# Optimization experiments

Hardware: AMD Instinct MI355X
Metric: run time of the kernel (lower is better)

## Reference

```python
import jax, jax.numpy as jnp
import numpy as np

DIM = 2048
N_HEADS = 16
KV_LORA = 512
NOPE = 128
ROPE = 64
V_DIM = 128
QK_DIM = NOPE + ROPE  # 192
B, S = 2, 2048
ROPE_THETA = 10000.0
ROPE_FACTOR = 40.0
BETA_FAST, BETA_SLOW = 32, 1
ORIG_LEN, MAX_LEN = 4096, 16384
MSCALE_ARG = 1.0
EPS = 1e-6


def _precompute_freqs(seqlen):
    # DeepSeek YaRN-corrected rotary frequencies (interleaved-pair convention).
    d = ROPE
    freqs = 1.0 / (ROPE_THETA ** (np.arange(0, d, 2, dtype=np.float64) / d))
    if MAX_LEN > ORIG_LEN:
        def corr_dim(n_rot):
            return d * np.log(ORIG_LEN / (n_rot * 2 * np.pi)) / (2 * np.log(ROPE_THETA))
        low = max(int(np.floor(corr_dim(BETA_FAST))), 0)
        high = min(int(np.ceil(corr_dim(BETA_SLOW))), d - 1)
        smooth = 1.0 - np.clip((np.arange(d // 2) - low) / max(high - low, 1e-3), 0, 1)
        freqs = freqs / ROPE_FACTOR * (1 - smooth) + freqs * smooth
    t = np.arange(seqlen, dtype=np.float64)
    ang = np.outer(t, freqs)  # [S, d/2]
    return np.cos(ang).astype(np.float32), np.sin(ang).astype(np.float32)


def softmax_scale():
    scale = QK_DIM ** -0.5
    if MAX_LEN > ORIG_LEN:
        m = 0.1 * MSCALE_ARG * float(np.log(ROPE_FACTOR)) + 1.0
        scale = scale * m * m
    return scale


def setup_inputs() -> dict:
    key = jax.random.key(0)
    ks = jax.random.split(key, 6)
    w_std = 0.02
    fc, fs = _precompute_freqs(S)
    return {
        "x": jax.random.normal(ks[0], (B, S, DIM), jnp.float32),
        "wq": jax.random.normal(ks[1], (N_HEADS * QK_DIM, DIM), jnp.float32) * w_std,
        "wkv_a": jax.random.normal(ks[2], (KV_LORA + ROPE, DIM), jnp.float32) * w_std,
        "kv_norm_w": jnp.ones((KV_LORA,), jnp.float32),
        "wkv_b": jax.random.normal(ks[3], (N_HEADS * (NOPE + V_DIM), KV_LORA), jnp.float32) * w_std,
        "wo": jax.random.normal(ks[4], (DIM, N_HEADS * V_DIM), jnp.float32) * w_std,
        "freqs_cos": jnp.asarray(fc),
        "freqs_sin": jnp.asarray(fs),
    }


def _apply_rotary(x, cos, sin):
    # x: [B, S, H, d]; interleaved complex pairs, cos/sin: [S, d/2]
    xr = x.reshape(*x.shape[:-1], -1, 2)
    x_re, x_im = xr[..., 0], xr[..., 1]
    c = cos[None, :, None, :]
    s = sin[None, :, None, :]
    y_re = x_re * c - x_im * s
    y_im = x_re * s + x_im * c
    return jnp.stack((y_re, y_im), axis=-1).reshape(x.shape)


def _rmsnorm(x, w):
    return x * jax.lax.rsqrt(jnp.mean(x * x, axis=-1, keepdims=True) + EPS) * w


def reference(x, wq, wkv_a, kv_norm_w, wkv_b, wo, freqs_cos, freqs_sin):
    b, s, _ = x.shape
    # Q projection (q_lora_rank == 0 path)
    q = (x @ wq.T).reshape(b, s, N_HEADS, QK_DIM)
    q_nope, q_pe = q[..., :NOPE], q[..., NOPE:]
    q_pe = _apply_rotary(q_pe, freqs_cos, freqs_sin)
    # Low-rank KV compression
    kv = x @ wkv_a.T  # [B, S, 512+64]
    kv_c, k_pe = kv[..., :KV_LORA], kv[..., KV_LORA:]
    k_pe = _apply_rotary(k_pe[:, :, None, :], freqs_cos, freqs_sin)  # [B,S,1,64]
    kv_c = _rmsnorm(kv_c, kv_norm_w)
    kvb = (kv_c @ wkv_b.T).reshape(b, s, N_HEADS, NOPE + V_DIM)
    k_nope, v = kvb[..., :NOPE], kvb[..., NOPE:]
    k = jnp.concatenate([k_nope, jnp.broadcast_to(k_pe, (b, s, N_HEADS, ROPE))], axis=-1)
    # Causal attention
    scores = jnp.einsum("bshd,bthd->bhst", q, k) * softmax_scale()
    causal = jnp.tril(jnp.ones((s, s), bool))
    scores = jnp.where(causal[None, None], scores, jnp.float32(-1e30))
    p = jax.nn.softmax(scores, axis=-1)
    out = jnp.einsum("bhst,bthd->bshd", p, v).reshape(b, s, N_HEADS * V_DIM)
    return out @ wo.T
```

## Files before the change

kernel.cpp:

```cpp
#include <hip/hip_runtime.h>
#include <math.h>

#define NH      16
#define D_NOPE  128
#define D_ROPE  64
#define D_QK    192
#define D_V     128
#define KV_LORA 512
#define NB      2
#define SEQ     2048
#define NTOK    (NB*SEQ)
#define QROW    (NH*D_QK)
#define KVBROW  (NH*(D_NOPE+D_V))
#define EPSF    1e-6f

typedef unsigned short u16;
typedef float  floatx4 __attribute__((ext_vector_type(4)));
typedef __bf16 bf16x8  __attribute__((ext_vector_type(8)));
typedef u16    u16x4   __attribute__((ext_vector_type(4)));
typedef u16    u16x8   __attribute__((ext_vector_type(8)));

__device__ __forceinline__ u16 f2bf(float f) {
    unsigned u = __builtin_bit_cast(unsigned, f);
    return (u16)((u + 0x7fffu + ((u >> 16) & 1u)) >> 16);
}

__device__ __forceinline__ void async_copy16(const void* g, void* l) {
    __builtin_amdgcn_global_load_lds(
        (const __attribute__((address_space(1))) unsigned int*)g,
        (__attribute__((address_space(3))) unsigned int*)l,
        16, 0, 0);
}

__global__ __launch_bounds__(256) void cast_bf16(const float* __restrict__ in,
                                                 u16* __restrict__ out) {
    const int i = (blockIdx.x * 256 + threadIdx.x) * 4;
    const float4 v = *(const float4*)&in[i];
    u16x4 o; o[0] = f2bf(v.x); o[1] = f2bf(v.y); o[2] = f2bf(v.z); o[3] = f2bf(v.w);
    *(u16x4*)&out[i] = o;
}

__global__ __launch_bounds__(256) void cast_pad_wkva(const float* __restrict__ in,
                                                     u16* __restrict__ out) {
    const int i = (blockIdx.x * 256 + threadIdx.x) * 4;
    const int r = i >> 11;
    u16x4 o;
    if (r < 576) {
        const float4 v = *(const float4*)&in[i];
        o[0] = f2bf(v.x); o[1] = f2bf(v.y); o[2] = f2bf(v.z); o[3] = f2bf(v.w);
    } else {
        o[0] = 0; o[1] = 0; o[2] = 0; o[3] = 0;
    }
    *(u16x4*)&out[i] = o;
}

template<int MODE>
__global__ __launch_bounds__(256) void gemm_mfma(const u16* __restrict__ A,
                                                 const u16* __restrict__ B,
                                                 void* __restrict__ Cout,
                                                 u16* __restrict__ kbuf,
                                                 u16* __restrict__ vT,
                                                 int M, int N, int K) {
    __shared__ u16 As[128 * 32];
    __shared__ u16 Bs[128 * 32];
    const int tid  = threadIdx.x;
    const int wave = tid >> 6, lane = tid & 63;
    const int m0 = blockIdx.y * 128, n0 = blockIdx.x * 128;
    const int wm = (wave & 1) * 64, wn = (wave >> 1) * 64;

    const int srow = wave * 32 + (lane >> 2);
    const int kch  = (lane & 3) * 8;
    const u16* gA0 = A + (size_t)(m0 + srow) * K + kch;
    const u16* gA1 = gA0 + (size_t)16 * K;
    const u16* gB0 = B + (size_t)(n0 + srow) * K + kch;
    const u16* gB1 = gB0 + (size_t)16 * K;
    u16* lA0 = &As[(wave * 32) * 32];
    u16* lA1 = &As[(wave * 32 + 16) * 32];
    u16* lB0 = &Bs[(wave * 32) * 32];
    u16* lB1 = &Bs[(wave * 32 + 16) * 32];

    floatx4 acc[4][4];
#pragma unroll
    for (int i = 0; i < 4; ++i)
#pragma unroll
        for (int j = 0; j < 4; ++j) acc[i][j] = 0.f;

    const int lrow = lane & 15;
    const int lkh  = (lane >> 4) * 8;

    for (int k0 = 0; k0 < K; k0 += 32) {
        __syncthreads();
        async_copy16(gA0 + k0, lA0);
        async_copy16(gA1 + k0, lA1);
        async_copy16(gB0 + k0, lB0);
        async_copy16(gB1 + k0, lB1);
        __syncthreads();
        bf16x8 a[4], b[4];
#pragma unroll
        for (int mi = 0; mi < 4; ++mi)
            a[mi] = *(const bf16x8*)&As[(wm + mi * 16 + lrow) * 32 + lkh];
#pragma unroll
        for (int ni = 0; ni < 4; ++ni)
            b[ni] = *(const bf16x8*)&Bs[(wn + ni * 16 + lrow) * 32 + lkh];
#pragma unroll
        for (int mi = 0; mi < 4; ++mi)
#pragma unroll
            for (int ni = 0; ni < 4; ++ni)
                acc[mi][ni] = __builtin_amdgcn_mfma_f32_16x16x32_bf16(
                    a[mi], b[ni], acc[mi][ni], 0, 0, 0);
    }

    const int crow = (lane >> 4) * 4, ccol = lane & 15;
#pragma unroll
    for (int mi = 0; mi < 4; ++mi)
#pragma unroll
        for (int ni = 0; ni < 4; ++ni) {
            const int m = m0 + wm + mi * 16 + crow;
            const int c = n0 + wn + ni * 16 + ccol;
            if (MODE == 0) {
                float* cp = (float*)Cout + (size_t)m * N + c;
#pragma unroll
                for (int r = 0; r < 4; ++r) cp[(size_t)r * N] = acc[mi][ni][r];
            } else if (MODE == 1) {
                u16* cp = (u16*)Cout + (size_t)m * N + c;
#pragma unroll
                for (int r = 0; r < 4; ++r) cp[(size_t)r * N] = f2bf(acc[mi][ni][r]);
            } else {
                const int hh = c >> 8, j = c & 255;
                const int bb = m >> 11, t = m & 2047;
                if (j < 128) {
#pragma unroll
                    for (int r = 0; r < 4; ++r)
                        kbuf[(((size_t)hh * 2 + bb) * 2048 + t + r) * 192 + j] =
                            f2bf(acc[mi][ni][r]);
                } else {
                    u16x4 pk;
#pragma unroll
                    for (int r = 0; r < 4; ++r) pk[r] = f2bf(acc[mi][ni][r]);
                    *(u16x4*)&vT[(((size_t)hh * 2 + bb) * 128 + (j - 128)) * 2048 + t] = pk;
                }
            }
        }
}


__global__ __launch_bounds__(256) void kv_fix(const float* __restrict__ kv_raw,
                                              const float* __restrict__ w,
                                              const float* __restrict__ fcos,
                                              const float* __restrict__ fsin,
                                              u16* __restrict__ kvn_bf,
                                              u16* __restrict__ kbuf) {
    const int row = blockIdx.x;
    const int tid = threadIdx.x;
    const float* src = kv_raw + (size_t)row * 640;
    const float v0 = src[tid];
    const float v1 = src[256 + tid];
    float ss = v0 * v0 + v1 * v1;
#pragma unroll
    for (int off = 32; off > 0; off >>= 1) ss += __shfl_down(ss, off, 64);
    __shared__ float red[4];
    __shared__ float kpe_s[64];
    if ((tid & 63) == 0) red[tid >> 6] = ss;
    if (tid < 32) {
        const int s = row & (SEQ - 1);
        const float c  = fcos[s * 32 + tid];
        const float sn = fsin[s * 32 + tid];
        const float xr = src[KV_LORA + 2 * tid];
        const float xi = src[KV_LORA + 2 * tid + 1];
        kpe_s[2 * tid]     = xr * c - xi * sn;
        kpe_s[2 * tid + 1] = xr * sn + xi * c;
    }
    __syncthreads();
    const float tot = red[0] + red[1] + red[2] + red[3];
    const float inv = rsqrtf(tot * (1.0f / KV_LORA) + EPSF);
    kvn_bf[(size_t)row * KV_LORA + tid]       = f2bf(v0 * inv * w[tid]);
    kvn_bf[(size_t)row * KV_LORA + 256 + tid] = f2bf(v1 * inv * w[256 + tid]);
    const int bb = row >> 11, t = row & 2047;
    const int hh = tid >> 4, dg = (tid & 15) * 4;
    u16x4 pk;
#pragma unroll
    for (int j = 0; j < 4; ++j) pk[j] = f2bf(kpe_s[dg + j]);
    *(u16x4*)&kbuf[(((size_t)hh * 2 + bb) * 2048 + t) * 192 + 128 + dg] = pk;
}

__global__ __launch_bounds__(256) void attn_mfma(const u16* __restrict__ qbf,
                                                 const u16* __restrict__ kbuf,
                                                 const u16* __restrict__ vT,
                                                 u16* __restrict__ att,
                                                 float scale) {
    __shared__ __attribute__((aligned(16))) u16 Ks[6 * 64 * 32];
    __shared__ __attribute__((aligned(16))) u16 Vs[2 * 128 * 32];
    __shared__ __attribute__((aligned(16))) u16 Ps[4][16 * 72];
    const int qt = blockIdx.x, h = blockIdx.y, b = blockIdx.z;
    const int tid = threadIdx.x, wave = tid >> 6, lane = tid & 63;
    const int l15 = lane & 15, lg = lane >> 4;

    const int qrow = qt * 64 + wave * 16 + l15;
    const size_t qoff = ((size_t)(b * SEQ + qrow)) * QROW + h * 192 + lg * 8;
    bf16x8 qf[6];
#pragma unroll
    for (int s = 0; s < 6; ++s) qf[s] = *(const bf16x8*)&qbf[qoff + s * 32];

    const u16* kb_base = kbuf + ((size_t)(h * 2 + b)) * 2048 * 192;
    const u16* vt_base = vT   + ((size_t)(h * 2 + b)) * 128 * 2048;

    floatx4 oacc[8];
#pragma unroll
    for (int v = 0; v < 8; ++v) oacc[v] = 0.f;
    float m_run = -1e30f, l_run = 0.f;

    for (int tt = 0; tt <= qt; ++tt) {
        const int t0 = tt * 64;
        __syncthreads();
#pragma unroll
        for (int i = 0; i < 6; ++i) {
            const int base = (wave * 6 + i) * 64;
            const int slot = base + lane;
            const int s = slot >> 8, r = slot & 255, tk = r >> 2, ch = r & 3;
            async_copy16(kb_base + ((size_t)(t0 + tk)) * 192 + s * 32 + ch * 8,
                         &Ks[base * 8]);
        }
#pragma unroll
        for (int i = 0; i < 4; ++i) {
            const int base = (wave * 4 + i) * 64;
            const int slot = base + lane;
            const int s = slot >> 9, r = slot & 511, v = r >> 2, ch = r & 3;
            async_copy16(vt_base + ((size_t)v) * 2048 + t0 + s * 32 + ch * 8,
                         &Vs[base * 8]);
        }
        __syncthreads();
        floatx4 sacc[4];
#pragma unroll
        for (int mt = 0; mt < 4; ++mt) sacc[mt] = 0.f;
#pragma unroll
        for (int s = 0; s < 6; ++s) {
#pragma unroll
            for (int mt = 0; mt < 4; ++mt) {
                const bf16x8 kf = *(const bf16x8*)&Ks[(s * 64 + mt * 16 + l15) * 32 + lg * 8];
                sacc[mt] = __builtin_amdgcn_mfma_f32_16x16x32_bf16(kf, qf[s], sacc[mt], 0, 0, 0);
            }
        }
        float p[16];
        float tmax = -1e30f;
#pragma unroll
        for (int mt = 0; mt < 4; ++mt)
#pragma unroll
            for (int r = 0; r < 4; ++r) {
                const int tglob = t0 + mt * 16 + lg * 4 + r;
                float v = sacc[mt][r] * scale;
                v = (tglob <= qrow) ? v : -1e30f;
                p[mt * 4 + r] = v;
                tmax = fmaxf(tmax, v);
            }
        tmax = fmaxf(tmax, __shfl_xor(tmax, 16));
        tmax = fmaxf(tmax, __shfl_xor(tmax, 32));
        const float mnew = fmaxf(m_run, tmax);
        const float alpha = __expf(m_run - mnew);
        m_run = mnew;
        float rsum = 0.f;
#pragma unroll
        for (int k = 0; k < 16; ++k) { p[k] = __expf(p[k] - mnew); rsum += p[k]; }
        rsum += __shfl_xor(rsum, 16);
        rsum += __shfl_xor(rsum, 32);
        l_run = l_run * alpha + rsum;
#pragma unroll
        for (int mt = 0; mt < 4; ++mt) {
            u16x4 pk;
#pragma unroll
            for (int r = 0; r < 4; ++r) pk[r] = f2bf(p[mt * 4 + r]);
            *(u16x4*)&Ps[wave][l15 * 72 + mt * 16 + lg * 4] = pk;
        }
        float af[4];
#pragma unroll
        for (int r = 0; r < 4; ++r) af[r] = __shfl(alpha, lg * 4 + r);
#pragma unroll
        for (int vt = 0; vt < 8; ++vt)
#pragma unroll
            for (int r = 0; r < 4; ++r) oacc[vt][r] *= af[r];
#pragma unroll
        for (int s = 0; s < 2; ++s) {
            const bf16x8 pf = *(const bf16x8*)&Ps[wave][l15 * 72 + s * 32 + lg * 8];
#pragma unroll
            for (int vt = 0; vt < 8; ++vt) {
                const bf16x8 vf = *(const bf16x8*)&Vs[(s * 128 + vt * 16 + l15) * 32 + lg * 8];
                oacc[vt] = __builtin_amdgcn_mfma_f32_16x16x32_bf16(pf, vf, oacc[vt], 0, 0, 0);
            }
        }
    }
    float lf[4];
#pragma unroll
    for (int r = 0; r < 4; ++r) lf[r] = 1.0f / __shfl(l_run, lg * 4 + r);
#pragma unroll
    for (int vt = 0; vt < 8; ++vt)
#pragma unroll
        for (int r = 0; r < 4; ++r) {
            const int orow = b * SEQ + qt * 64 + wave * 16 + lg * 4 + r;
            att[(size_t)orow * 2048 + h * 128 + vt * 16 + l15] = f2bf(oacc[vt][r] * lf[r]);
        }
}

extern "C" void kernel_launch(void* const* d_in, const int* in_sizes, int n_in,
                              void* d_out, int out_size, void* d_ws, size_t ws_size,
                              hipStream_t stream) {
    const float* x     = (const float*)d_in[0];
    const float* wq    = (const float*)d_in[1];
    const float* wkv_a = (const float*)d_in[2];
    const float* knw   = (const float*)d_in[3];
    const float* wkv_b = (const float*)d_in[4];
    const float* wo    = (const float*)d_in[5];
    const float* fcos  = (const float*)d_in[6];
    const float* fsin  = (const float*)d_in[7];
    float* out = (float*)d_out;

    char* w = (char*)d_ws;
    u16*   x_bf    = (u16*)w;  w += (size_t)NTOK * 2048 * 2;
    u16*   wq_bf   = (u16*)w;  w += (size_t)QROW * 2048 * 2;
    u16*   wkva_bf = (u16*)w;  w += (size_t)640 * 2048 * 2;
    u16*   wkvb_bf = (u16*)w;  w += (size_t)KVBROW * KV_LORA * 2;
    u16*   wo_bf   = (u16*)w;  w += (size_t)2048 * 2048 * 2;
    u16*   q_bf    = (u16*)w;  w += (size_t)NTOK * QROW * 2;
    float* kv_raw  = (float*)w; w += (size_t)NTOK * 640 * 4;
    u16*   kvn_bf  = (u16*)w;  w += (size_t)NTOK * KV_LORA * 2;
    u16*   kbuf    = (u16*)w;  w += (size_t)NH * NB * SEQ * 192 * 2;
    u16*   vT      = (u16*)w;  w += (size_t)NH * NB * 128 * SEQ * 2;
    u16*   att_bf  = (u16*)w;  w += (size_t)NTOK * 2048 * 2;

    const double mm = 0.1 * 1.0 * log(40.0) + 1.0;
    const float scale = (float)((1.0 / sqrt((double)D_QK)) * mm * mm);

    dim3 blk(256);
    cast_bf16<<<dim3(NTOK * 2048 / 1024), blk, 0, stream>>>(x, x_bf);
    cast_bf16<<<dim3(QROW * 2048 / 1024), blk, 0, stream>>>(wq, wq_bf);
    cast_pad_wkva<<<dim3(640 * 2048 / 1024), blk, 0, stream>>>(wkv_a, wkva_bf);
    cast_bf16<<<dim3(KVBROW * KV_LORA / 1024), blk, 0, stream>>>(wkv_b, wkvb_bf);
    cast_bf16<<<dim3(2048 * 2048 / 1024), blk, 0, stream>>>(wo, wo_bf);
    gemm_mfma<1><<<dim3(QROW / 128, NTOK / 128), blk, 0, stream>>>(
        x_bf, wq_bf, q_bf, nullptr, nullptr, NTOK, QROW, 2048);
    gemm_mfma<0><<<dim3(640 / 128, NTOK / 128), blk, 0, stream>>>(
        x_bf, wkva_bf, kv_raw, nullptr, nullptr, NTOK, 640, 2048);
    kv_fix<<<dim3(NTOK), blk, 0, stream>>>(kv_raw, knw, fcos, fsin, kvn_bf, kbuf);
    gemm_mfma<2><<<dim3(KVBROW / 128, NTOK / 128), blk, 0, stream>>>(
        kvn_bf, wkvb_bf, nullptr, kbuf, vT, NTOK, KVBROW, KV_LORA);
    attn_mfma<<<dim3(SEQ / 64, NH, NB), blk, 0, stream>>>(q_bf, kbuf, vT, att_bf, scale);
    gemm_mfma<0><<<dim3(2048 / 128, NTOK / 128), blk, 0, stream>>>(
        att_bf, wo_bf, out, nullptr, nullptr, NTOK, 2048, 2048);
}
```

Before: 511.2 us.

## Process two query groups per attention block to reuse K/V tiles

```diff
diff --git a/kernel.cpp b/kernel.cpp
--- a/kernel.cpp
+++ b/kernel.cpp
@@ -183,34 +183,42 @@
     *(u16x4*)&kbuf[(((size_t)hh * 2 + bb) * 2048 + t) * 192 + 128 + dg] = pk;
 }
 
-__global__ __launch_bounds__(256) void attn_mfma(const u16* __restrict__ qbf,
-                                                 const u16* __restrict__ kbuf,
-                                                 const u16* __restrict__ vT,
-                                                 u16* __restrict__ att,
-                                                 float scale) {
+__global__ __launch_bounds__(256, 2) void attn_mfma(const u16* __restrict__ qbf,
+                                                    const u16* __restrict__ kbuf,
+                                                    const u16* __restrict__ vT,
+                                                    u16* __restrict__ att,
+                                                    float scale) {
     __shared__ __attribute__((aligned(16))) u16 Ks[6 * 64 * 32];
     __shared__ __attribute__((aligned(16))) u16 Vs[2 * 128 * 32];
-    __shared__ __attribute__((aligned(16))) u16 Ps[4][16 * 72];
-    const int qt = blockIdx.x, h = blockIdx.y, b = blockIdx.z;
+    __shared__ __attribute__((aligned(16))) u16 Ps[4][32 * 72];
+    const int qt = (gridDim.x - 1) - blockIdx.x;
+    const int h = blockIdx.y, b = blockIdx.z;
     const int tid = threadIdx.x, wave = tid >> 6, lane = tid & 63;
     const int l15 = lane & 15, lg = lane >> 4;
 
-    const int qrow = qt * 64 + wave * 16 + l15;
-    const size_t qoff = ((size_t)(b * SEQ + qrow)) * QROW + h * 192 + lg * 8;
-    bf16x8 qf[6];
-#pragma unroll
-    for (int s = 0; s < 6; ++s) qf[s] = *(const bf16x8*)&qbf[qoff + s * 32];
+    int qrow[2];
+    bf16x8 qf[2][6];
+#pragma unroll
+    for (int g = 0; g < 2; ++g) {
+        qrow[g] = qt * 128 + g * 64 + wave * 16 + l15;
+        const size_t qoff = ((size_t)(b * SEQ + qrow[g])) * QROW + h * 192 + lg * 8;
+#pragma unroll
+        for (int s = 0; s < 6; ++s) qf[g][s] = *(const bf16x8*)&qbf[qoff + s * 32];
+    }
 
     const u16* kb_base = kbuf + ((size_t)(h * 2 + b)) * 2048 * 192;
     const u16* vt_base = vT   + ((size_t)(h * 2 + b)) * 128 * 2048;
 
-    floatx4 oacc[8];
-#pragma unroll
-    for (int v = 0; v < 8; ++v) oacc[v] = 0.f;
-    float m_run = -1e30f, l_run = 0.f;
-
-    for (int tt = 0; tt <= qt; ++tt) {
-        const int t0 = tt * 64;
+    floatx4 oacc[2][8];
+#pragma unroll
+    for (int g = 0; g < 2; ++g)
+#pragma unroll
+        for (int v = 0; v < 8; ++v) oacc[g][v] = 0.f;
+    float m_run[2] = {-1e30f, -1e30f}, l_run[2] = {0.f, 0.f};
+
+    const int kt_max = 2 * qt + 1;
+    for (int kt = 0; kt <= kt_max; ++kt) {
+        const int t0 = kt * 64;
         __syncthreads();
 #pragma unroll
         for (int i = 0; i < 6; ++i) {
@@ -229,74 +237,96 @@
                          &Vs[base * 8]);
         }
         __syncthreads();
-        floatx4 sacc[4];
-#pragma unroll
-        for (int mt = 0; mt < 4; ++mt) sacc[mt] = 0.f;
+        floatx4 sacc[2][4];
+#pragma unroll
+        for (int g = 0; g < 2; ++g)
+#pragma unroll
+            for (int mt = 0; mt < 4; ++mt) sacc[g][mt] = 0.f;
 #pragma unroll
         for (int s = 0; s < 6; ++s) {
 #pragma unroll
             for (int mt = 0; mt < 4; ++mt) {
                 const bf16x8 kf = *(const bf16x8*)&Ks[(s * 64 + mt * 16 + l15) * 32 + lg * 8];
-                sacc[mt] = __builtin_amdgcn_mfma_f32_16x16x32_bf16(kf, qf[s], sacc[mt], 0, 0, 0);
-            }
-        }
-        float p[16];
-        float tmax = -1e30f;
-#pragma unroll
-        for (int mt = 0; mt < 4; ++mt)
-#pragma unroll
-            for (int r = 0; r < 4; ++r) {
-                const int tglob = t0 + mt * 16 + lg * 4 + r;
-                float v = sacc[mt][r] * scale;
-                v = (tglob <= qrow) ? v : -1e30f;
-                p[mt * 4 + r] = v;
-                tmax = fmaxf(tmax, v);
-            }
-        tmax = fmaxf(tmax, __shfl_xor(tmax, 16));
-        tmax = fmaxf(tmax, __shfl_xor(tmax, 32));
-        const float mnew = fmaxf(m_run, tmax);
-        const float alpha = __expf(m_run - mnew);
-        m_run = mnew;
-        float rsum = 0.f;
-#pragma unroll
-        for (int k = 0; k < 16; ++k) { p[k] = __expf(p[k] - mnew); rsum += p[k]; }
-        rsum += __shfl_xor(rsum, 16);
-        rsum += __shfl_xor(rsum, 32);
-        l_run = l_run * alpha + rsum;
-#pragma unroll
-        for (int mt = 0; mt < 4; ++mt) {
-            u16x4 pk;
-#pragma unroll
-            for (int r = 0; r < 4; ++r) pk[r] = f2bf(p[mt * 4 + r]);
-            *(u16x4*)&Ps[wave][l15 * 72 + mt * 16 + lg * 4] = pk;
-        }
-        float af[4];
-#pragma unroll
-        for (int r = 0; r < 4; ++r) af[r] = __shfl(alpha, lg * 4 + r);
-#pragma unroll
-        for (int vt = 0; vt < 8; ++vt)
-#pragma unroll
-            for (int r = 0; r < 4; ++r) oacc[vt][r] *= af[r];
+#pragma unroll
+                for (int g = 0; g < 2; ++g)
+                    sacc[g][mt] = __builtin_amdgcn_mfma_f32_16x16x32_bf16(
+                        kf, qf[g][s], sacc[g][mt], 0, 0, 0);
+            }
+        }
+        float alpha[2];
+#pragma unroll
+        for (int g = 0; g < 2; ++g) {
+            float p[16];
+            float tmax = -1e30f;
+#pragma unroll
+            for (int mt = 0; mt < 4; ++mt)
+#pragma unroll
+                for (int r = 0; r < 4; ++r) {
+                    const int tglob = t0 + mt * 16 + lg * 4 + r;
+                    float v = sacc[g][mt][r] * scale;
+                    v = (tglob <= qrow[g]) ? v : -1e30f;
+                    p[mt * 4 + r] = v;
+                    tmax = fmaxf(tmax, v);
+                }
+            tmax = fmaxf(tmax, __shfl_xor(tmax, 16));
+            tmax = fmaxf(tmax, __shfl_xor(tmax, 32));
+            const float mnew = fmaxf(m_run[g], tmax);
+            alpha[g] = __expf(m_run[g] - mnew);
+            m_run[g] = mnew;
+            float rsum = 0.f;
+#pragma unroll
+            for (int k = 0; k < 16; ++k) { p[k] = __expf(p[k] - mnew); rsum += p[k]; }
+            rsum += __shfl_xor(rsum, 16);
+            rsum += __shfl_xor(rsum, 32);
+            l_run[g] = l_run[g] * alpha[g] + rsum;
+#pragma unroll
+            for (int mt = 0; mt < 4; ++mt) {
+                u16x4 pk;
+#pragma unroll
+                for (int r = 0; r < 4; ++r) pk[r] = f2bf(p[mt * 4 + r]);
+                *(u16x4*)&Ps[wave][(g * 16 + l15) * 72 + mt * 16 + lg * 4] = pk;
+            }
+        }
+#pragma unroll
+        for (int g = 0; g < 2; ++g) {
+            float af[4];
+#pragma unroll
+            for (int r = 0; r < 4; ++r) af[r] = __shfl(alpha[g], lg * 4 + r);
+#pragma unroll
+            for (int vt = 0; vt < 8; ++vt)
+#pragma unroll
+                for (int r = 0; r < 4; ++r) oacc[g][vt][r] *= af[r];
+        }
 #pragma unroll
         for (int s = 0; s < 2; ++s) {
-            const bf16x8 pf = *(const bf16x8*)&Ps[wave][l15 * 72 + s * 32 + lg * 8];
+            bf16x8 pf[2];
+#pragma unroll
+            for (int g = 0; g < 2; ++g)
+                pf[g] = *(const bf16x8*)&Ps[wave][(g * 16 + l15) * 72 + s * 32 + lg * 8];
 #pragma unroll
             for (int vt = 0; vt < 8; ++vt) {
                 const bf16x8 vf = *(const bf16x8*)&Vs[(s * 128 + vt * 16 + l15) * 32 + lg * 8];
-                oacc[vt] = __builtin_amdgcn_mfma_f32_16x16x32_bf16(pf, vf, oacc[vt], 0, 0, 0);
-            }
-        }
-    }
-    float lf[4];
-#pragma unroll
-    for (int r = 0; r < 4; ++r) lf[r] = 1.0f / __shfl(l_run, lg * 4 + r);
-#pragma unroll
-    for (int vt = 0; vt < 8; ++vt)
-#pragma unroll
-        for (int r = 0; r < 4; ++r) {
-            const int orow = b * SEQ + qt * 64 + wave * 16 + lg * 4 + r;
-            att[(size_t)orow * 2048 + h * 128 + vt * 16 + l15] = f2bf(oacc[vt][r] * lf[r]);
-        }
+#pragma unroll
+                for (int g = 0; g < 2; ++g)
+                    oacc[g][vt] = __builtin_amdgcn_mfma_f32_16x16x32_bf16(
+                        pf[g], vf, oacc[g][vt], 0, 0, 0);
+            }
+        }
+    }
+#pragma unroll
+    for (int g = 0; g < 2; ++g) {
+        float lf[4];
+#pragma unroll
+        for (int r = 0; r < 4; ++r) lf[r] = 1.0f / __shfl(l_run[g], lg * 4 + r);
+#pragma unroll
+        for (int vt = 0; vt < 8; ++vt)
+#pragma unroll
+            for (int r = 0; r < 4; ++r) {
+                const int orow = b * SEQ + qt * 128 + g * 64 + wave * 16 + lg * 4 + r;
+                att[(size_t)orow * 2048 + h * 128 + vt * 16 + l15] =
+                    f2bf(oacc[g][vt][r] * lf[r]);
+            }
+    }
 }
 
 extern "C" void kernel_launch(void* const* d_in, const int* in_sizes, int n_in,
@@ -341,7 +371,7 @@
     kv_fix<<<dim3(NTOK), blk, 0, stream>>>(kv_raw, knw, fcos, fsin, kvn_bf, kbuf);
     gemm_mfma<2><<<dim3(KVBROW / 128, NTOK / 128), blk, 0, stream>>>(
         kvn_bf, wkvb_bf, nullptr, kbuf, vT, NTOK, KVBROW, KV_LORA);
-    attn_mfma<<<dim3(SEQ / 64, NH, NB), blk, 0, stream>>>(q_bf, kbuf, vT, att_bf, scale);
+    attn_mfma<<<dim3(SEQ / 128, NH, NB), blk, 0, stream>>>(q_bf, kbuf, vT, att_bf, scale);
     gemm_mfma<0><<<dim3(2048 / 128, NTOK / 128), blk, 0, stream>>>(
         att_bf, wo_bf, out, nullptr, nullptr, NTOK, 2048, 2048);
 }
```

Result: faster. 476.0 us (-6.9%).
